# Kernel tuning notes

Hardware: AMD Instinct MI355X
Metric: run time of the kernel (lower is better)

## Reference

```python
import jax, jax.numpy as jnp
import numpy as np

B, L, M = 4, 16384, 256
HID, FDIM, INNER, ODIM = 512, 128, 128, 3
HEADS, DH = 2, 64
NFREQ = 16  # feature_dim // (2 * input_dim)
ALPHA = 10.0
SIGMA_Q = 128.0
SIGMA_LS = (128.0, 32.0, 8.0)


def setup_inputs() -> dict:
    key = jax.random.key(0)
    ks = jax.random.split(key, 16)
    s = 0.02
    nl = len(SIGMA_LS)
    return {
        "x": jax.random.uniform(ks[0], (B, L, 4), jnp.float32),
        "tokens": jax.random.normal(ks[1], (B, M, HID), jnp.float32),
        "w_query": jax.random.normal(ks[2], (FDIM, HID), jnp.float32) * s,
        "b_query": jnp.zeros((HID,), jnp.float32),
        "w_to_q": jax.random.normal(ks[3], (HID, INNER), jnp.float32) * s,
        "w_to_kv": jax.random.normal(ks[4], (HID, 2 * INNER), jnp.float32) * s,
        "w_to_out": jax.random.normal(ks[5], (INNER, HID), jnp.float32) * s,
        "b_to_out": jnp.zeros((HID,), jnp.float32),
        "w_band": jax.random.normal(ks[6], (nl, FDIM, HID), jnp.float32) * s,
        "b_band": jnp.zeros((nl, HID), jnp.float32),
        "w_mod": jax.random.normal(ks[7], (nl, HID, HID), jnp.float32) * s,
        "b_mod": jnp.zeros((nl, HID), jnp.float32),
        "w_hv": jax.random.normal(ks[8], (nl - 1, HID, HID), jnp.float32) * s,
        "b_hv": jnp.zeros((nl - 1, HID), jnp.float32),
        "w_out": jax.random.normal(ks[9], (nl, HID, ODIM), jnp.float32) * s,
        "b_out": jnp.zeros((nl, ODIM), jnp.float32),
        "Dd": 8, "Hh": 16, "Ww": 16, "Tt": 8,
    }


def _calc_gamma(grid, omegas):
    # grid: [L, 4]; omegas: [NFREQ] -> gamma: [L, 4*2*NFREQ] = [L, FDIM]
    arg = jnp.pi * grid[:, :, None] * omegas[None, None, :]
    return jnp.concatenate([jnp.sin(arg), jnp.cos(arg)], axis=-1).reshape(grid.shape[0], -1)


def reference(x, tokens, w_query, b_query, w_to_q, w_to_kv, w_to_out, b_to_out,
              w_band, b_band, w_mod, b_mod, w_hv, b_hv, w_out, b_out, Dd, Hh, Ww, Tt):
    Bn, Ln, _ = x.shape
    m = tokens.shape[1]
    grid = x[0]  # grid shared across batch, exactly as in the torch module (uses x[0])

    # relative-position bias (ALiBi-like) from approximate patch indices
    z_i = (grid[:, 0] * Dd).astype(jnp.int32)
    y_i = (grid[:, 1] * Hh).astype(jnp.int32)
    x_i = (grid[:, 2] * Ww).astype(jnp.int32)
    t_i = (grid[:, 3] * Tt).astype(jnp.int32)
    idx = ((t_i * Dd + z_i) * Hh + y_i) * Ww + x_i  # [L]
    n_tot = Dd * Hh * Ww * Tt
    t = idx.astype(jnp.float32) / n_tot
    tok_pos = (jnp.arange(m, dtype=jnp.float32) + 0.5) / m
    bias = -ALPHA * (t[:, None] - tok_pos[None, :]) ** 2  # [L, m]

    # Fourier-feature query path (shared across batch)
    omegas_q = jnp.logspace(1.0, np.log10(SIGMA_Q), NFREQ, dtype=jnp.float32)
    x_q = jax.nn.relu(_calc_gamma(grid, omegas_q) @ w_query + b_query)  # [L, HID]

    # cross attention with additive bias
    q = (x_q @ w_to_q).reshape(Ln, HEADS, DH).transpose(1, 0, 2)  # [H, L, Dh]
    kv = tokens @ w_to_kv  # [B, m, 2*INNER]
    k, v = jnp.split(kv, 2, axis=-1)
    k = k.reshape(Bn, m, HEADS, DH).transpose(0, 2, 1, 3)  # [B, H, m, Dh]
    v = v.reshape(Bn, m, HEADS, DH).transpose(0, 2, 1, 3)
    sim = jnp.einsum('hld,bhmd->bhlm', q, k) * (DH ** -0.5) + bias[None, None]
    attn = jax.nn.softmax(sim, axis=-1)
    out = jnp.einsum('bhlm,bhmd->bhld', attn, v)
    out = out.transpose(0, 2, 1, 3).reshape(Bn, Ln, HEADS * DH)
    modv = out @ w_to_out + b_to_out  # [B, L, HID]

    # modulated MLP chain with residual hv accumulation
    total = jnp.zeros((Bn, Ln, w_out.shape[-1]), dtype=x.dtype)
    hv = None
    for kk in range(len(SIGMA_LS)):
        omg = jnp.logspace(1.0, np.log10(SIGMA_LS[kk]), NFREQ, dtype=jnp.float32)
        h_l = jax.nn.relu(_calc_gamma(grid, omg) @ w_band[kk] + b_band[kk])  # [L, HID]
        m_l = jax.nn.relu(h_l[None] + modv @ w_mod[kk] + b_mod[kk])  # [B, L, HID]
        if kk == 0:
            hv = m_l
        else:
            hv = jax.nn.relu((m_l + hv) @ w_hv[kk - 1] + b_hv[kk - 1])
        total = total + hv @ w_out[kk] + b_out[kk]
    return total  # [B, L, ODIM]
```

## Files before the change

kernel.cpp:

```cpp
#include <hip/hip_runtime.h>

#define L_N   16384
#define B_N   4
#define M_N   256
#define HID_N 512
#define PI_F  3.14159265358979323846f

typedef short short8 __attribute__((ext_vector_type(8)));
typedef float f32x4 __attribute__((ext_vector_type(4)));

__device__ __forceinline__ ushort f2bf(float f) {
  uint u = __float_as_uint(f);
  uint r = u + 0x7FFF + ((u >> 16) & 1);
  return (ushort)(r >> 16);
}
__device__ __forceinline__ float bf2f(ushort s) {
  return __uint_as_float(((uint)s) << 16);
}
__device__ __forceinline__ void gld_lds16(const void* g, void* s) {
  __builtin_amdgcn_global_load_lds((const __attribute__((address_space(1))) void*)g,
                                   (__attribute__((address_space(3))) void*)s, 16, 0, 0);
}

__global__ __launch_bounds__(256) void k_wt_all(
    const float* __restrict__ w_query, const float* __restrict__ w_to_q,
    const float* __restrict__ w_to_kv, const float* __restrict__ w_to_out,
    const float* __restrict__ w_band, const float* __restrict__ w_mod,
    const float* __restrict__ w_hv,
    ushort* __restrict__ wq_t, ushort* __restrict__ wtq_t,
    ushort* __restrict__ wkv_t, ushort* __restrict__ wto_t,
    ushort* __restrict__ wb_t, ushort* __restrict__ wm_t, ushort* __restrict__ whv_t) {
  __shared__ float t[32][33];
  int tb = blockIdx.x;
  const float* in; ushort* out; int R, C;
  if (tb < 64)        { in = w_query;  out = wq_t;  R = 128; C = 512; }
  else if (tb < 128)  { tb -= 64;  in = w_to_q;   out = wtq_t; R = 512; C = 128; }
  else if (tb < 256)  { tb -= 128; in = w_to_kv;  out = wkv_t; R = 512; C = 256; }
  else if (tb < 320)  { tb -= 256; in = w_to_out; out = wto_t; R = 128; C = 512; }
  else if (tb < 512)  { tb -= 320; int kk = tb >> 6; tb &= 63;
                        in = w_band + (size_t)kk * 65536; out = wb_t + (size_t)kk * 65536; R = 128; C = 512; }
  else if (tb < 1280) { tb -= 512; int kk = tb >> 8; tb &= 255;
                        in = w_mod + (size_t)kk * 262144; out = wm_t + (size_t)kk * 262144; R = 512; C = 512; }
  else                { tb -= 1280; int kk = tb >> 8; tb &= 255;
                        in = w_hv + (size_t)kk * 262144; out = whv_t + (size_t)kk * 262144; R = 512; C = 512; }
  int nbx = C >> 5;
  int bx = (tb % nbx) * 32, by = (tb / nbx) * 32;
  int tx = threadIdx.x & 31, ty = threadIdx.x >> 5;
#pragma unroll
  for (int j = 0; j < 32; j += 8) t[ty + j][tx] = in[(size_t)(by + ty + j) * C + bx + tx];
  __syncthreads();
#pragma unroll
  for (int j = 0; j < 32; j += 8)
    out[(size_t)(bx + ty + j) * R + by + tx] = f2bf(t[tx][ty + j]);
}

__global__ __launch_bounds__(256) void k_cvt(const float* __restrict__ in,
                                             ushort* __restrict__ out, int n4) {
  int i = blockIdx.x * 256 + threadIdx.x;
  if (i >= n4) return;
  float4 v = *(const float4*)&in[(size_t)i * 4];
  ushort* o = &out[(size_t)i * 4];
  o[0] = f2bf(v.x); o[1] = f2bf(v.y); o[2] = f2bf(v.z); o[3] = f2bf(v.w);
}

__global__ __launch_bounds__(256) void k_gamma(const float* __restrict__ x,
                                               ushort* __restrict__ gout) {
  __shared__ float om[16];
  const float lgs[4] = {2.1072099696478683f, 2.1072099696478683f,
                        1.5051499783199058f, 0.9030899869919435f};
  int spec = blockIdx.y;
  float lg = lgs[spec];
  int tid = threadIdx.x;
  if (tid < 16) om[tid] = powf(10.0f, 1.0f + (float)tid * ((lg - 1.0f) * (1.0f / 15.0f)));
  __syncthreads();
  int l0 = blockIdx.x * 16;
  int idx0 = tid * 8;
  int row = idx0 >> 7, f0 = idx0 & 127;
  int c = f0 >> 5;
  float g = x[(size_t)(l0 + row) * 4 + c];
  float base = PI_F * g;
  int w0 = f0 & 31;
  bool is_cos = (w0 >= 16);
  short8 o;
#pragma unroll
  for (int j = 0; j < 8; ++j) {
    int jf = (w0 + j) & 15;
    float arg = base * om[jf];
    float v = is_cos ? __cosf(arg) : __sinf(arg);
    o[j] = (short)f2bf(v);
  }
  *(short8*)&gout[(size_t)spec * L_N * 128 + (size_t)(l0 + row) * 128 + f0] = o;
}

__global__ __launch_bounds__(256) void k_tpos(const float* __restrict__ x,
                                              const int* dD, const int* dH,
                                              const int* dW, const int* dT,
                                              float* __restrict__ tbuf) {
  int l = blockIdx.x * 256 + threadIdx.x;
  float g0 = x[(size_t)l * 4 + 0], g1 = x[(size_t)l * 4 + 1];
  float g2 = x[(size_t)l * 4 + 2], g3 = x[(size_t)l * 4 + 3];
  int Dd = dD[0], Hh = dH[0], Ww = dW[0], Tt = dT[0];
  int zi = (int)(g0 * (float)Dd), yi = (int)(g1 * (float)Hh);
  int xi = (int)(g2 * (float)Ww), ti = (int)(g3 * (float)Tt);
  int idx = ((ti * Dd + zi) * Hh + yi) * Ww + xi;
  tbuf[l] = (float)idx / (float)(Dd * Hh * Ww * Tt);
}

__global__ __launch_bounds__(256, 4) void k_gemm2(
    const ushort* __restrict__ A, long long sA,
    const ushort* __restrict__ Wt, long long sWt,
    const float* __restrict__ bias, int sBias,
    const ushort* __restrict__ add1,
    const ushort* add2, long long sAdd2,
    ushort* C, long long sC,
    const float* __restrict__ wout,
    float* __restrict__ opb,
    int zoff,
    int N, int K, int do_relu,
    int nbx, int nby, int nz) {
  __shared__ __align__(16) ushort S[128 * 64 * 2];
  __shared__ float woutL[384];
  ushort* As = S;
  ushort* Ws = S + 128 * 64;
  int tid = threadIdx.x;
  int lane = tid & 63, wid = tid >> 6;

  int nwg = nbx * nby * nz;
  int gid0 = blockIdx.x;
  int q = nwg >> 3, r = nwg & 7;
  int xcd = gid0 & 7, rank = gid0 >> 3;
  int sid = (xcd < r) ? (xcd * (q + 1) + rank) : (r * (q + 1) + (xcd - r) * q + rank);
  int z = sid / (nbx * nby);
  int rem = sid - z * (nbx * nby);
  int n0 = (rem % nbx) * 128, r0 = (rem / nbx) * 128;

  A += (size_t)z * sA;
  ushort* Cp = C ? C + (size_t)z * sC : nullptr;
  const ushort* Wtp = Wt + (size_t)z * sWt;
  const float* biasp = bias ? bias + (size_t)z * sBias : nullptr;
  const ushort* a2p = add2 ? add2 + (size_t)z * sAdd2 : nullptr;
  int wr = wid >> 1, wc = wid & 1;
  int ksm = K >> 6;

  f32x4 acc[4][4];
#pragma unroll
  for (int i = 0; i < 4; ++i)
#pragma unroll
    for (int j = 0; j < 4; ++j) acc[i][j] = (f32x4)0.0f;

  for (int t = 0; t < ksm; ++t) {
#pragma unroll
    for (int j = 0; j < 4; ++j) {
      int sig = j * 256 + wid * 64 + lane;
      int rr = sig >> 3, ph = sig & 7, sl = ph ^ (rr & 7);
      gld_lds16(&A[(size_t)(r0 + rr) * K + t * 64 + sl * 8], &As[(size_t)(j * 256 + wid * 64) * 8]);
      gld_lds16(&Wtp[(size_t)(n0 + rr) * K + t * 64 + sl * 8], &Ws[(size_t)(j * 256 + wid * 64) * 8]);
    }
    __syncthreads();
#pragma unroll
    for (int ks = 0; ks < 2; ++ks) {
      short8 af[4], bg[4];
#pragma unroll
      for (int fm = 0; fm < 4; ++fm) {
        int row = wr * 64 + fm * 16 + (lane & 15);
        af[fm] = *(const short8*)&As[row * 64 + (((ks * 4 + (lane >> 4)) ^ (row & 7)) * 8)];
      }
#pragma unroll
      for (int fn = 0; fn < 4; ++fn) {
        int nl = wc * 64 + fn * 16 + (lane & 15);
        bg[fn] = *(const short8*)&Ws[nl * 64 + (((ks * 4 + (lane >> 4)) ^ (nl & 7)) * 8)];
      }
#pragma unroll
      for (int fm = 0; fm < 4; ++fm)
#pragma unroll
        for (int fn = 0; fn < 4; ++fn)
          acc[fm][fn] = __builtin_amdgcn_mfma_f32_16x16x32_bf16(af[fm], bg[fn], acc[fm][fn], 0, 0, 0);
    }
    __syncthreads();
  }

  if (wout && tid < 128) {
    woutL[tid * 3 + 0] = wout[(size_t)(n0 + tid) * 3 + 0];
    woutL[tid * 3 + 1] = wout[(size_t)(n0 + tid) * 3 + 1];
    woutL[tid * 3 + 2] = wout[(size_t)(n0 + tid) * 3 + 2];
  }

  float* Ls = (float*)S;
  int row = tid >> 3;
  int c0 = (tid & 7) * 16;
#pragma unroll
  for (int fm = 0; fm < 4; ++fm) {
    if (fm) __syncthreads();
#pragma unroll
    for (int fn = 0; fn < 4; ++fn)
#pragma unroll
      for (int reg = 0; reg < 4; ++reg) {
        int lr = wr * 16 + (lane >> 4) * 4 + reg;
        int lc = wc * 64 + fn * 16 + (lane & 15);
        Ls[lr * 132 + lc] = acc[fm][fn][reg];
      }
    __syncthreads();
    int gr = r0 + (row >> 4) * 64 + fm * 16 + (row & 15);
    float so0 = 0.0f, so1 = 0.0f, so2 = 0.0f;
#pragma unroll
    for (int hh = 0; hh < 2; ++hh) {
      int cc = c0 + hh * 8;
      float v[8];
#pragma unroll
      for (int j = 0; j < 8; ++j) v[j] = Ls[row * 132 + cc + j];
      if (biasp) {
#pragma unroll
        for (int j = 0; j < 8; ++j) v[j] += biasp[n0 + cc + j];
      }
      if (add1) {
        short8 a1 = *(const short8*)&add1[(size_t)gr * N + n0 + cc];
#pragma unroll
        for (int j = 0; j < 8; ++j) v[j] += bf2f((ushort)a1[j]);
      }
      if (do_relu) {
#pragma unroll
        for (int j = 0; j < 8; ++j) v[j] = fmaxf(v[j], 0.0f);
      }
      if (a2p) {
        short8 a2 = *(const short8*)&a2p[(size_t)gr * N + n0 + cc];
#pragma unroll
        for (int j = 0; j < 8; ++j) v[j] += bf2f((ushort)a2[j]);
      }
      if (wout) {
#pragma unroll
        for (int j = 0; j < 8; ++j) {
          so0 = fmaf(v[j], woutL[(cc + j) * 3 + 0], so0);
          so1 = fmaf(v[j], woutL[(cc + j) * 3 + 1], so1);
          so2 = fmaf(v[j], woutL[(cc + j) * 3 + 2], so2);
        }
      }
      if (Cp) {
        short8 ov;
#pragma unroll
        for (int j = 0; j < 8; ++j) ov[j] = (short)f2bf(v[j]);
        *(short8*)&Cp[(size_t)gr * N + n0 + cc] = ov;
      }
    }
    if (wout) {
      so0 += __shfl_down(so0, 4); so1 += __shfl_down(so1, 4); so2 += __shfl_down(so2, 4);
      so0 += __shfl_down(so0, 2); so1 += __shfl_down(so1, 2); so2 += __shfl_down(so2, 2);
      so0 += __shfl_down(so0, 1); so1 += __shfl_down(so1, 1); so2 += __shfl_down(so2, 1);
      if ((tid & 7) == 0) {
        int bx = n0 >> 7;
        size_t oi = (((size_t)bx * 4 + (zoff + z)) * L_N + gr) * 3;
        opb[oi + 0] += so0; opb[oi + 1] += so1; opb[oi + 2] += so2;
      }
    }
  }
}

__global__ __launch_bounds__(256, 2) void k_mpair(
    const ushort* __restrict__ modv,
    const ushort* __restrict__ wm_t,
    const float* __restrict__ b_mod,
    const ushort* __restrict__ hband,
    const float* __restrict__ wout,
    float* __restrict__ opb, int zoff,
    ushort* __restrict__ s1,
    int nbx, int nby, int nz) {
  __shared__ __align__(16) ushort S[3 * 128 * 64];
  __shared__ float woutL[384];
  const size_t big = (size_t)L_N * HID_N;
  ushort* As = S;
  ushort* W0 = S + 128 * 64;
  ushort* W1 = S + 2 * 128 * 64;
  int tid = threadIdx.x;
  int lane = tid & 63, wid = tid >> 6;

  int nwg = nbx * nby * nz;
  int gid0 = blockIdx.x;
  int q = nwg >> 3, r = nwg & 7;
  int xcd = gid0 & 7, rank = gid0 >> 3;
  int sid = (xcd < r) ? (xcd * (q + 1) + rank) : (r * (q + 1) + (xcd - r) * q + rank);
  int z = sid / (nbx * nby);
  int rem = sid - z * (nbx * nby);
  int n0 = (rem % nbx) * 128, r0 = (rem / nbx) * 128;

  const ushort* A = modv + (size_t)z * big;
  ushort* Cp = s1 + (size_t)z * big;
  int wr = wid >> 1, wc = wid & 1;

  f32x4 acc0[4][4], acc1[4][4];
#pragma unroll
  for (int i = 0; i < 4; ++i)
#pragma unroll
    for (int j = 0; j < 4; ++j) { acc0[i][j] = (f32x4)0.0f; acc1[i][j] = (f32x4)0.0f; }

  for (int t = 0; t < 8; ++t) {
#pragma unroll
    for (int j = 0; j < 4; ++j) {
      int sig = j * 256 + wid * 64 + lane;
      int rr = sig >> 3, ph = sig & 7, sl = ph ^ (rr & 7);
      gld_lds16(&A[(size_t)(r0 + rr) * 512 + t * 64 + sl * 8], &As[(size_t)sig * 8]);
      gld_lds16(&wm_t[(size_t)(n0 + rr) * 512 + t * 64 + sl * 8], &W0[(size_t)sig * 8]);
      gld_lds16(&wm_t[262144 + (size_t)(n0 + rr) * 512 + t * 64 + sl * 8], &W1[(size_t)sig * 8]);
    }
    __syncthreads();
#pragma unroll
    for (int ks = 0; ks < 2; ++ks) {
      short8 af[4], bg0[4], bg1[4];
#pragma unroll
      for (int fm = 0; fm < 4; ++fm) {
        int rrow = wr * 64 + fm * 16 + (lane & 15);
        af[fm] = *(const short8*)&As[rrow * 64 + (((ks * 4 + (lane >> 4)) ^ (rrow & 7)) * 8)];
      }
#pragma unroll
      for (int fn = 0; fn < 4; ++fn) {
        int nl = wc * 64 + fn * 16 + (lane & 15);
        int off = nl * 64 + (((ks * 4 + (lane >> 4)) ^ (nl & 7)) * 8);
        bg0[fn] = *(const short8*)&W0[off];
        bg1[fn] = *(const short8*)&W1[off];
      }
#pragma unroll
      for (int fm = 0; fm < 4; ++fm)
#pragma unroll
        for (int fn = 0; fn < 4; ++fn) {
          acc0[fm][fn] = __builtin_amdgcn_mfma_f32_16x16x32_bf16(af[fm], bg0[fn], acc0[fm][fn], 0, 0, 0);
          acc1[fm][fn] = __builtin_amdgcn_mfma_f32_16x16x32_bf16(af[fm], bg1[fn], acc1[fm][fn], 0, 0, 0);
        }
    }
    __syncthreads();
  }

  if (tid < 128) {
    woutL[tid * 3 + 0] = wout[(size_t)(n0 + tid) * 3 + 0];
    woutL[tid * 3 + 1] = wout[(size_t)(n0 + tid) * 3 + 1];
    woutL[tid * 3 + 2] = wout[(size_t)(n0 + tid) * 3 + 2];
  }

  float* Ls0 = (float*)S;
  float* Ls1 = (float*)S + 32 * 132;
  int row = tid >> 3;
  int c0 = (tid & 7) * 16;
#pragma unroll
  for (int fm = 0; fm < 4; ++fm) {
    if (fm) __syncthreads();
#pragma unroll
    for (int fn = 0; fn < 4; ++fn)
#pragma unroll
      for (int reg = 0; reg < 4; ++reg) {
        int lr = wr * 16 + (lane >> 4) * 4 + reg;
        int lc = wc * 64 + fn * 16 + (lane & 15);
        Ls0[lr * 132 + lc] = acc0[fm][fn][reg];
        Ls1[lr * 132 + lc] = acc1[fm][fn][reg];
      }
    __syncthreads();
    int gr = r0 + (row >> 4) * 64 + fm * 16 + (row & 15);
    float so0 = 0.0f, so1 = 0.0f, so2 = 0.0f;
#pragma unroll
    for (int hh = 0; hh < 2; ++hh) {
      int cc = c0 + hh * 8;
      short8 h0 = *(const short8*)&hband[(size_t)gr * 512 + n0 + cc];
      short8 h1 = *(const short8*)&hband[big + (size_t)gr * 512 + n0 + cc];
      float v0[8], v1[8];
#pragma unroll
      for (int j = 0; j < 8; ++j) {
        v0[j] = fmaxf(Ls0[row * 132 + cc + j] + b_mod[n0 + cc + j] + bf2f((ushort)h0[j]), 0.0f);
        v1[j] = fmaxf(Ls1[row * 132 + cc + j] + b_mod[512 + n0 + cc + j] + bf2f((ushort)h1[j]), 0.0f);
        so0 = fmaf(v0[j], woutL[(cc + j) * 3 + 0], so0);
        so1 = fmaf(v0[j], woutL[(cc + j) * 3 + 1], so1);
        so2 = fmaf(v0[j], woutL[(cc + j) * 3 + 2], so2);
      }
      short8 ov;
#pragma unroll
      for (int j = 0; j < 8; ++j) ov[j] = (short)f2bf(v0[j] + v1[j]);
      *(short8*)&Cp[(size_t)gr * 512 + n0 + cc] = ov;
    }
    so0 += __shfl_down(so0, 4); so1 += __shfl_down(so1, 4); so2 += __shfl_down(so2, 4);
    so0 += __shfl_down(so0, 2); so1 += __shfl_down(so1, 2); so2 += __shfl_down(so2, 2);
    so0 += __shfl_down(so0, 1); so1 += __shfl_down(so1, 1); so2 += __shfl_down(so2, 1);
    if ((tid & 7) == 0) {
      int bx = n0 >> 7;
      size_t oi = (((size_t)bx * 4 + (zoff + z)) * L_N + gr) * 3;
      opb[oi + 0] = so0; opb[oi + 1] = so1; opb[oi + 2] = so2;
    }
  }
}

__global__ __launch_bounds__(256) void k_outred(const float* __restrict__ opb,
                                                const float* __restrict__ b_out,
                                                float* __restrict__ out) {
  int i = blockIdx.x * 256 + threadIdx.x;
  if (i >= B_N * L_N) return;
  float a0 = b_out[0] + b_out[3] + b_out[6];
  float a1 = b_out[1] + b_out[4] + b_out[7];
  float a2 = b_out[2] + b_out[5] + b_out[8];
#pragma unroll
  for (int bx = 0; bx < 4; ++bx) {
    const float* p = opb + ((size_t)bx * 4 * L_N + i) * 3;
    a0 += p[0]; a1 += p[1]; a2 += p[2];
  }
  out[(size_t)i * 3 + 0] = a0;
  out[(size_t)i * 3 + 1] = a1;
  out[(size_t)i * 3 + 2] = a2;
}

__global__ __launch_bounds__(256) void k_rearr(const ushort* __restrict__ kvtmp,
                                               ushort* __restrict__ kbuf,
                                               ushort* __restrict__ vtb) {
  int i = blockIdx.x * 256 + threadIdx.x;
  int col = i & 255, row = i >> 8;
  int b = row >> 8, m = row & 255;
  ushort v = kvtmp[i];
  if (col < 128)
    kbuf[((size_t)b * 256 + m) * 128 + col] = v;
  else
    vtb[(size_t)b * 128 * 256 + (size_t)(col - 128) * 256 + m] = v;
}

__global__ __launch_bounds__(256) void k_attn_m(const ushort* __restrict__ qbuf,
                                                const float* __restrict__ tbuf,
                                                const ushort* __restrict__ kbuf,
                                                const ushort* __restrict__ vtb,
                                                ushort* __restrict__ attn) {
  __shared__ __align__(16) ushort Kt[256 * 64];
  __shared__ __align__(16) ushort Vt[64 * 256];
  __shared__ __align__(16) ushort Qs[64 * 64];
  __shared__ __align__(16) ushort Pw[4][16 * 40];
  __shared__ float ts[64];
  int tid = threadIdx.x;
  int lane = tid & 63, wid = tid >> 6;
  int l0 = blockIdx.x * 64;
  int h = blockIdx.y;
  int z = blockIdx.z;
  const ushort* kbuf_b = kbuf + (size_t)z * M_N * 128;
  const ushort* vtb_b = vtb + (size_t)z * 128 * M_N;
  ushort* attn_b = attn + (size_t)z * L_N * 128;
#pragma unroll
  for (int j = 0; j < 8; ++j) {
    int sig = j * 256 + wid * 64 + lane;
    int m = sig >> 3, ph = sig & 7, sl = ph ^ (m & 7);
    gld_lds16(&kbuf_b[(size_t)m * 128 + h * 64 + sl * 8], &Kt[(size_t)(j * 256 + wid * 64) * 8]);
  }
#pragma unroll
  for (int j = 0; j < 8; ++j) {
    int sig = j * 256 + wid * 64 + lane;
    int d = sig >> 5, ph = sig & 31, sl = ph ^ ((d & 7) << 2);
    gld_lds16(&vtb_b[(size_t)(h * 64 + d) * 256 + sl * 8], &Vt[(size_t)(j * 256 + wid * 64) * 8]);
  }
#pragma unroll
  for (int j = 0; j < 2; ++j) {
    int sig = j * 256 + wid * 64 + lane;
    int qq = sig >> 3, ph = sig & 7, sl = ph ^ (qq & 7);
    gld_lds16(&qbuf[(size_t)(l0 + qq) * 128 + h * 64 + sl * 8], &Qs[(size_t)(j * 256 + wid * 64) * 8]);
  }
  if (tid < 64) ts[tid] = tbuf[l0 + tid];
  __syncthreads();

  f32x4 s_acc[16];
#pragma unroll
  for (int fn = 0; fn < 16; ++fn) s_acc[fn] = (f32x4)0.0f;
#pragma unroll
  for (int ks = 0; ks < 2; ++ks) {
    int qrow = wid * 16 + (lane & 15);
    short8 aq = *(const short8*)&Qs[qrow * 64 + (((ks * 4 + (lane >> 4)) ^ (qrow & 7)) * 8)];
#pragma unroll
    for (int fn = 0; fn < 16; ++fn) {
      int m = fn * 16 + (lane & 15);
      short8 bk = *(const short8*)&Kt[m * 64 + (((ks * 4 + (lane >> 4)) ^ (m & 7)) * 8)];
      s_acc[fn] = __builtin_amdgcn_mfma_f32_16x16x32_bf16(aq, bk, s_acc[fn], 0, 0, 0);
    }
  }
  float mx[4] = {-1e30f, -1e30f, -1e30f, -1e30f};
#pragma unroll
  for (int fn = 0; fn < 16; ++fn) {
#pragma unroll
    for (int reg = 0; reg < 4; ++reg) {
      int ql = wid * 16 + (lane >> 4) * 4 + reg;
      int m = fn * 16 + (lane & 15);
      float mp = ((float)m + 0.5f) * (1.0f / 256.0f);
      float d = ts[ql] - mp;
      float v = s_acc[fn][reg] * 0.125f - 10.0f * d * d;
      s_acc[fn][reg] = v;
      mx[reg] = fmaxf(mx[reg], v);
    }
  }
#pragma unroll
  for (int reg = 0; reg < 4; ++reg) {
    mx[reg] = fmaxf(mx[reg], __shfl_xor(mx[reg], 1));
    mx[reg] = fmaxf(mx[reg], __shfl_xor(mx[reg], 2));
    mx[reg] = fmaxf(mx[reg], __shfl_xor(mx[reg], 4));
    mx[reg] = fmaxf(mx[reg], __shfl_xor(mx[reg], 8));
  }
  float sm[4] = {0.0f, 0.0f, 0.0f, 0.0f};
#pragma unroll
  for (int fn = 0; fn < 16; ++fn) {
#pragma unroll
    for (int reg = 0; reg < 4; ++reg) {
      float e = __expf(s_acc[fn][reg] - mx[reg]);
      s_acc[fn][reg] = e;
      sm[reg] += e;
    }
  }
#pragma unroll
  for (int reg = 0; reg < 4; ++reg) {
    sm[reg] += __shfl_xor(sm[reg], 1);
    sm[reg] += __shfl_xor(sm[reg], 2);
    sm[reg] += __shfl_xor(sm[reg], 4);
    sm[reg] += __shfl_xor(sm[reg], 8);
  }
  float inv[4];
#pragma unroll
  for (int reg = 0; reg < 4; ++reg) inv[reg] = 1.0f / sm[reg];

  f32x4 o_acc[4];
#pragma unroll
  for (int fn = 0; fn < 4; ++fn) o_acc[fn] = (f32x4)0.0f;
  for (int kk = 0; kk < 8; ++kk) {
#pragma unroll
    for (int fp = 0; fp < 2; ++fp) {
      int fn = kk * 2 + fp;
#pragma unroll
      for (int reg = 0; reg < 4; ++reg) {
        int ql16 = (lane >> 4) * 4 + reg;
        int mc = fp * 16 + (lane & 15);
        Pw[wid][ql16 * 40 + mc] = f2bf(s_acc[fn][reg] * inv[reg]);
      }
    }
    asm volatile("s_waitcnt lgkmcnt(0)" ::: "memory");
    __builtin_amdgcn_sched_barrier(0);
    short8 pa = *(const short8*)&Pw[wid][(lane & 15) * 40 + (lane >> 4) * 8];
#pragma unroll
    for (int fn = 0; fn < 4; ++fn) {
      int dr = fn * 16 + (lane & 15);
      short8 vb = *(const short8*)&Vt[dr * 256 + (((kk * 4 + (lane >> 4)) ^ ((dr & 7) << 2)) * 8)];
      o_acc[fn] = __builtin_amdgcn_mfma_f32_16x16x32_bf16(pa, vb, o_acc[fn], 0, 0, 0);
    }
    asm volatile("s_waitcnt lgkmcnt(0)" ::: "memory");
    __builtin_amdgcn_sched_barrier(0);
  }
#pragma unroll
  for (int fn = 0; fn < 4; ++fn)
#pragma unroll
    for (int reg = 0; reg < 4; ++reg) {
      int ql = l0 + wid * 16 + (lane >> 4) * 4 + reg;
      attn_b[(size_t)ql * 128 + h * 64 + fn * 16 + (lane & 15)] = f2bf(o_acc[fn][reg]);
    }
}

extern "C" void kernel_launch(void* const* d_in, const int* in_sizes, int n_in,
                              void* d_out, int out_size, void* d_ws, size_t ws_size,
                              hipStream_t stream) {
  const float* x        = (const float*)d_in[0];
  const float* tokens   = (const float*)d_in[1];
  const float* w_query  = (const float*)d_in[2];
  const float* b_query  = (const float*)d_in[3];
  const float* w_to_q   = (const float*)d_in[4];
  const float* w_to_kv  = (const float*)d_in[5];
  const float* w_to_out = (const float*)d_in[6];
  const float* b_to_out = (const float*)d_in[7];
  const float* w_band   = (const float*)d_in[8];
  const float* b_band   = (const float*)d_in[9];
  const float* w_mod    = (const float*)d_in[10];
  const float* b_mod    = (const float*)d_in[11];
  const float* w_hv     = (const float*)d_in[12];
  const float* b_hv     = (const float*)d_in[13];
  const float* w_out    = (const float*)d_in[14];
  const float* b_out    = (const float*)d_in[15];
  const int* Dd = (const int*)d_in[16];
  const int* Hh = (const int*)d_in[17];
  const int* Ww = (const int*)d_in[18];
  const int* Tt = (const int*)d_in[19];
  float* out = (float*)d_out;

  ushort* W = (ushort*)d_ws;
  size_t o = 0;
  auto alloc = [&](size_t n) { ushort* p = W + o; o += n; return p; };
  const size_t big = (size_t)L_N * HID_N;
  const size_t LQ = (size_t)L_N * 128;

  ushort* qb     = alloc(LQ);
  ushort* tokb   = alloc((size_t)B_N * M_N * HID_N);
  ushort* kbuf   = alloc((size_t)B_N * M_N * 128);
  ushort* vtb    = alloc((size_t)B_N * 128 * M_N);
  ushort* wq_t   = alloc(512 * 128);
  ushort* wtq_t  = alloc(128 * 512);
  ushort* wkv_t  = alloc(256 * 512);
  ushort* wto_t  = alloc(512 * 128);
  ushort* wb_t   = alloc(3 * 512 * 128);
  ushort* wm_t   = alloc(3 * 512 * 512);
  ushort* whv_t  = alloc(2 * 512 * 512);
  float* tbuf    = (float*)alloc(L_N * 2);
  size_t base_u = o;

  int NZ;
  if (ws_size >= (base_u + 15 * big) * sizeof(ushort)) NZ = 4;
  else if (ws_size >= (base_u + 10 * big) * sizeof(ushort)) NZ = 2;
  else NZ = 1;

  ushort *gammaR, *attnout, *s1, *hband, *modv, *hv1;
  if (NZ == 4) {
    gammaR  = alloc(4 * big);
    attnout = alloc(4 * big);
    hband   = alloc(3 * big);
    modv    = alloc(4 * big);
    hv1 = gammaR;
    s1  = attnout;
  } else {
    gammaR  = alloc((size_t)(NZ > 1 ? NZ : 1) * big);
    attnout = alloc(big);
    s1      = alloc((size_t)NZ * big);
    hband   = alloc(3 * big);
    modv    = alloc((size_t)NZ * big);
    hv1 = gammaR;
  }
  ushort* xq = modv;
  ushort* kvtmp = attnout;
  float* opb = (float*)qb;

  const long long BG = (long long)big;
  const long long LQs = (long long)LQ;

  k_wt_all<<<dim3(1792), 256, 0, stream>>>(w_query, w_to_q, w_to_kv, w_to_out, w_band, w_mod, w_hv,
                                           wq_t, wtq_t, wkv_t, wto_t, wb_t, wm_t, whv_t);
  k_cvt<<<dim3(512), 256, 0, stream>>>(tokens, tokb, B_N * M_N * HID_N / 4);
  k_gamma<<<dim3(L_N / 16, 4), 256, 0, stream>>>(x, gammaR);
  k_tpos<<<dim3(L_N / 256), 256, 0, stream>>>(x, Dd, Hh, Ww, Tt, tbuf);

  k_gemm2<<<dim3(4 * 128), 256, 0, stream>>>(gammaR, 0, wq_t, 0, b_query, 0, nullptr, nullptr, 0,
                                             xq, 0, nullptr, nullptr, 0, 512, 128, 1, 4, 128, 1);
  k_gemm2<<<dim3(1 * 128), 256, 0, stream>>>(xq, 0, wtq_t, 0, nullptr, 0, nullptr, nullptr, 0,
                                             qb, 0, nullptr, nullptr, 0, 128, 512, 0, 1, 128, 1);
  k_gemm2<<<dim3(2 * 8), 256, 0, stream>>>(tokb, 0, wkv_t, 0, nullptr, 0, nullptr, nullptr, 0,
                                           kvtmp, 0, nullptr, nullptr, 0, 256, 512, 0, 2, 8, 1);
  k_rearr<<<dim3(1024), 256, 0, stream>>>(kvtmp, kbuf, vtb);
  k_attn_m<<<dim3(L_N / 64, 2, 4), 256, 0, stream>>>(qb, tbuf, kbuf, vtb, attnout);
  k_gemm2<<<dim3(4 * 128 * 3), 256, 0, stream>>>(gammaR + LQ, LQs, wb_t, 65536, b_band, 512,
                                                 nullptr, nullptr, 0, hband, BG,
                                                 nullptr, nullptr, 0, 512, 128, 1, 4, 128, 3);

  for (int zoff = 0; zoff < B_N; zoff += NZ) {
    k_gemm2<<<dim3(4 * 128 * NZ), 256, 0, stream>>>(attnout + (size_t)zoff * LQ, LQs, wto_t, 0,
                                                    b_to_out, 0, nullptr, nullptr, 0,
                                                    modv, BG, nullptr, nullptr, 0,
                                                    512, 128, 0, 4, 128, NZ);
    k_mpair<<<dim3(4 * 128 * NZ), 256, 0, stream>>>(modv, wm_t, b_mod, hband, w_out,
                                                    opb, zoff, s1, 4, 128, NZ);
    k_gemm2<<<dim3(4 * 128 * NZ), 256, 0, stream>>>(s1, BG, whv_t, 0, b_hv, 0, nullptr, nullptr, 0,
                                                    hv1, BG, w_out + 1536, opb, zoff,
                                                    512, 512, 1, 4, 128, NZ);
    k_gemm2<<<dim3(4 * 128 * NZ), 256, 0, stream>>>(modv, BG, wm_t + 2 * 262144, 0, b_mod + 1024, 0,
                                                    hband + 2 * big, hv1, BG,
                                                    s1, BG, nullptr, nullptr, 0,
                                                    512, 512, 1, 4, 128, NZ);
    k_gemm2<<<dim3(4 * 128 * NZ), 256, 0, stream>>>(s1, BG, whv_t + 262144, 0, b_hv + 512, 0,
                                                    nullptr, nullptr, 0, nullptr, 0,
                                                    w_out + 3072, opb, zoff,
                                                    512, 512, 1, 4, 128, NZ);
  }
  k_outred<<<dim3((B_N * L_N + 255) / 256), 256, 0, stream>>>(opb, b_out, out);
}
```

Measured before the change: 393.6 us.

## Load GEMM operand fragments directly from global memory instead of staging through LDS

Both MFMA GEMM kernels (k_gemm2 and k_mpair) drop the global-to-LDS staging of A and weight tiles and their barriers. Each lane now reads its short8 fragments straight from global memory at per-lane base pointers, and shared memory is kept only for the epilogue. This removes LDS traffic and __syncthreads from the K loop and shrinks the LDS footprint, which may allow more resident blocks. In exchange, tiles are no longer shared through LDS, so each wave re-fetches overlapping data from L2/global. The loads are 16-byte strided row reads with no explicit prefetch or double buffering, which risks memory-latency stalls.

Result: slower. 827.0 us (+110.1%).

```diff
diff --git a/kernel.cpp b/kernel.cpp
--- a/kernel.cpp
+++ b/kernel.cpp
@@ -118,10 +118,8 @@
     int zoff,
     int N, int K, int do_relu,
     int nbx, int nby, int nz) {
-  __shared__ __align__(16) ushort S[128 * 64 * 2];
+  __shared__ __align__(16) float Ls[32 * 132];
   __shared__ float woutL[384];
-  ushort* As = S;
-  ushort* Ws = S + 128 * 64;
   int tid = threadIdx.x;
   int lane = tid & 63, wid = tid >> 6;
 
@@ -142,6 +140,14 @@
   int wr = wid >> 1, wc = wid & 1;
   int ksm = K >> 6;
 
+  const ushort* Abase[4];
+  const ushort* Wbase[4];
+#pragma unroll
+  for (int f = 0; f < 4; ++f) {
+    Abase[f] = A + (size_t)(r0 + wr * 64 + f * 16 + (lane & 15)) * K + (lane >> 4) * 8;
+    Wbase[f] = Wtp + (size_t)(n0 + wc * 64 + f * 16 + (lane & 15)) * K + (lane >> 4) * 8;
+  }
+
   f32x4 acc[4][4];
 #pragma unroll
   for (int i = 0; i < 4; ++i)
@@ -150,33 +156,19 @@
 
   for (int t = 0; t < ksm; ++t) {
 #pragma unroll
-    for (int j = 0; j < 4; ++j) {
-      int sig = j * 256 + wid * 64 + lane;
-      int rr = sig >> 3, ph = sig & 7, sl = ph ^ (rr & 7);
-      gld_lds16(&A[(size_t)(r0 + rr) * K + t * 64 + sl * 8], &As[(size_t)(j * 256 + wid * 64) * 8]);
-      gld_lds16(&Wtp[(size_t)(n0 + rr) * K + t * 64 + sl * 8], &Ws[(size_t)(j * 256 + wid * 64) * 8]);
-    }
-    __syncthreads();
-#pragma unroll
     for (int ks = 0; ks < 2; ++ks) {
+      int ko = t * 64 + ks * 32;
       short8 af[4], bg[4];
 #pragma unroll
-      for (int fm = 0; fm < 4; ++fm) {
-        int row = wr * 64 + fm * 16 + (lane & 15);
-        af[fm] = *(const short8*)&As[row * 64 + (((ks * 4 + (lane >> 4)) ^ (row & 7)) * 8)];
-      }
-#pragma unroll
-      for (int fn = 0; fn < 4; ++fn) {
-        int nl = wc * 64 + fn * 16 + (lane & 15);
-        bg[fn] = *(const short8*)&Ws[nl * 64 + (((ks * 4 + (lane >> 4)) ^ (nl & 7)) * 8)];
-      }
+      for (int f = 0; f < 4; ++f) af[f] = *(const short8*)(Abase[f] + ko);
+#pragma unroll
+      for (int f = 0; f < 4; ++f) bg[f] = *(const short8*)(Wbase[f] + ko);
 #pragma unroll
       for (int fm = 0; fm < 4; ++fm)
 #pragma unroll
         for (int fn = 0; fn < 4; ++fn)
           acc[fm][fn] = __builtin_amdgcn_mfma_f32_16x16x32_bf16(af[fm], bg[fn], acc[fm][fn], 0, 0, 0);
     }
-    __syncthreads();
   }
 
   if (wout && tid < 128) {
@@ -185,7 +177,6 @@
     woutL[tid * 3 + 2] = wout[(size_t)(n0 + tid) * 3 + 2];
   }
 
-  float* Ls = (float*)S;
   int row = tid >> 3;
   int c0 = (tid & 7) * 16;
 #pragma unroll
@@ -263,12 +254,9 @@
     float* __restrict__ opb, int zoff,
     ushort* __restrict__ s1,
     int nbx, int nby, int nz) {
-  __shared__ __align__(16) ushort S[3 * 128 * 64];
+  __shared__ __align__(16) float LsP[2][32 * 132];
   __shared__ float woutL[384];
   const size_t big = (size_t)L_N * HID_N;
-  ushort* As = S;
-  ushort* W0 = S + 128 * 64;
-  ushort* W1 = S + 2 * 128 * 64;
   int tid = threadIdx.x;
   int lane = tid & 63, wid = tid >> 6;
 
@@ -285,6 +273,16 @@
   ushort* Cp = s1 + (size_t)z * big;
   int wr = wid >> 1, wc = wid & 1;
 
+  const ushort* Abase[4];
+  const ushort* W0base[4];
+  const ushort* W1base[4];
+#pragma unroll
+  for (int f = 0; f < 4; ++f) {
+    Abase[f]  = A + (size_t)(r0 + wr * 64 + f * 16 + (lane & 15)) * 512 + (lane >> 4) * 8;
+    W0base[f] = wm_t + (size_t)(n0 + wc * 64 + f * 16 + (lane & 15)) * 512 + (lane >> 4) * 8;
+    W1base[f] = W0base[f] + 262144;
+  }
+
   f32x4 acc0[4][4], acc1[4][4];
 #pragma unroll
   for (int i = 0; i < 4; ++i)
@@ -293,29 +291,15 @@
 
   for (int t = 0; t < 8; ++t) {
 #pragma unroll
-    for (int j = 0; j < 4; ++j) {
-      int sig = j * 256 + wid * 64 + lane;
-      int rr = sig >> 3, ph = sig & 7, sl = ph ^ (rr & 7);
-      gld_lds16(&A[(size_t)(r0 + rr) * 512 + t * 64 + sl * 8], &As[(size_t)sig * 8]);
-      gld_lds16(&wm_t[(size_t)(n0 + rr) * 512 + t * 64 + sl * 8], &W0[(size_t)sig * 8]);
-      gld_lds16(&wm_t[262144 + (size_t)(n0 + rr) * 512 + t * 64 + sl * 8], &W1[(size_t)sig * 8]);
-    }
-    __syncthreads();
-#pragma unroll
     for (int ks = 0; ks < 2; ++ks) {
+      int ko = t * 64 + ks * 32;
       short8 af[4], bg0[4], bg1[4];
 #pragma unroll
-      for (int fm = 0; fm < 4; ++fm) {
-        int rrow = wr * 64 + fm * 16 + (lane & 15);
-        af[fm] = *(const short8*)&As[rrow * 64 + (((ks * 4 + (lane >> 4)) ^ (rrow & 7)) * 8)];
-      }
-#pragma unroll
-      for (int fn = 0; fn < 4; ++fn) {
-        int nl = wc * 64 + fn * 16 + (lane & 15);
-        int off = nl * 64 + (((ks * 4 + (lane >> 4)) ^ (nl & 7)) * 8);
-        bg0[fn] = *(const short8*)&W0[off];
-        bg1[fn] = *(const short8*)&W1[off];
-      }
+      for (int f = 0; f < 4; ++f) af[f] = *(const short8*)(Abase[f] + ko);
+#pragma unroll
+      for (int f = 0; f < 4; ++f) bg0[f] = *(const short8*)(W0base[f] + ko);
+#pragma unroll
+      for (int f = 0; f < 4; ++f) bg1[f] = *(const short8*)(W1base[f] + ko);
 #pragma unroll
       for (int fm = 0; fm < 4; ++fm)
 #pragma unroll
@@ -324,7 +308,6 @@
           acc1[fm][fn] = __builtin_amdgcn_mfma_f32_16x16x32_bf16(af[fm], bg1[fn], acc1[fm][fn], 0, 0, 0);
         }
     }
-    __syncthreads();
   }
 
   if (tid < 128) {
@@ -333,8 +316,6 @@
     woutL[tid * 3 + 2] = wout[(size_t)(n0 + tid) * 3 + 2];
   }
 
-  float* Ls0 = (float*)S;
-  float* Ls1 = (float*)S + 32 * 132;
   int row = tid >> 3;
   int c0 = (tid & 7) * 16;
 #pragma unroll
@@ -346,8 +327,8 @@
       for (int reg = 0; reg < 4; ++reg) {
         int lr = wr * 16 + (lane >> 4) * 4 + reg;
         int lc = wc * 64 + fn * 16 + (lane & 15);
-        Ls0[lr * 132 + lc] = acc0[fm][fn][reg];
-        Ls1[lr * 132 + lc] = acc1[fm][fn][reg];
+        LsP[0][lr * 132 + lc] = acc0[fm][fn][reg];
+        LsP[1][lr * 132 + lc] = acc1[fm][fn][reg];
       }
     __syncthreads();
     int gr = r0 + (row >> 4) * 64 + fm * 16 + (row & 15);
@@ -360,8 +341,8 @@
       float v0[8], v1[8];
 #pragma unroll
       for (int j = 0; j < 8; ++j) {
-        v0[j] = fmaxf(Ls0[row * 132 + cc + j] + b_mod[n0 + cc + j] + bf2f((ushort)h0[j]), 0.0f);
-        v1[j] = fmaxf(Ls1[row * 132 + cc + j] + b_mod[512 + n0 + cc + j] + bf2f((ushort)h1[j]), 0.0f);
+        v0[j] = fmaxf(LsP[0][row * 132 + cc + j] + b_mod[n0 + cc + j] + bf2f((ushort)h0[j]), 0.0f);
+        v1[j] = fmaxf(LsP[1][row * 132 + cc + j] + b_mod[512 + n0 + cc + j] + bf2f((ushort)h1[j]), 0.0f);
         so0 = fmaf(v0[j], woutL[(cc + j) * 3 + 0], so0);
         so1 = fmaf(v0[j], woutL[(cc + j) * 3 + 1], so1);
         so2 = fmaf(v0[j], woutL[(cc + j) * 3 + 2], so2);
```
